# Kernel optimization log

Hardware: AMD Instinct MI355X
Metric: run time of the kernel (lower is better)

## Reference

```python
import jax, jax.numpy as jnp
import numpy as np
import math

C = 768          # in_channels
KC = 768         # key_channels
VC = 768         # value_channels
H = 12           # head_count
B, N = 8, 2048


def setup_inputs() -> dict:
    key = jax.random.key(0)
    ks = jax.random.split(key, 9)
    s = 0.02
    return {
        "x": jax.random.normal(ks[0], (B, N, C), dtype=jnp.float32),
        # Linear weights stored as (in, out); y = x @ W + b
        "Wq": jax.random.normal(ks[1], (C, KC), dtype=jnp.float32) * s,
        "bq": jnp.zeros((KC,), dtype=jnp.float32),
        "Wk": jax.random.normal(ks[2], (C, KC), dtype=jnp.float32) * s,
        "bk": jnp.zeros((KC,), dtype=jnp.float32),
        "Wv": jax.random.normal(ks[3], (C, VC), dtype=jnp.float32) * s,
        "bv": jnp.zeros((VC,), dtype=jnp.float32),
        "Wr": jax.random.normal(ks[4], (VC, C), dtype=jnp.float32) * s,
        "br": jnp.zeros((C,), dtype=jnp.float32),
    }


def reference(x, Wq, bq, Wk, bk, Wv, bv, Wr, br):
    b, n, c = x.shape
    dk = KC // H  # head key channels
    dv = VC // H  # head value channels
    q = (x @ Wq + bq).reshape(b, n, H, dk)
    k = (x @ Wk + bk).reshape(b, n, H, dk)
    v = (x @ Wv + bv).reshape(b, n, H, dv)
    # NOTE: original scales by sqrt(N) (sequence length), not sqrt(d_head)
    scores = jnp.einsum("bqhd,bkhd->bhqk", q, k) / math.sqrt(n)
    attn = jax.nn.softmax(scores, axis=-1)
    out = jnp.einsum("bhqk,bkhd->bqhd", attn, v).reshape(b, n, VC)
    # reprojection + relu; dropout is identity in eval mode
    return jax.nn.relu(out @ Wr + br)
```

## Files before the change

### kernel.cpp

```cpp
#include <hip/hip_runtime.h>
#include <math.h>

typedef unsigned short u16;
typedef short short8 __attribute__((ext_vector_type(8)));
typedef float f32x4 __attribute__((ext_vector_type(4)));

#define BATCH 8
#define SEQ   2048
#define CH    768
#define NH    12
#define DH    64
#define BH    (BATCH*NH)
#define MTOT  (BATCH*SEQ)

#if __has_builtin(__builtin_amdgcn_exp2f)
#define EXP2F(x) __builtin_amdgcn_exp2f(x)
#else
#define EXP2F(x) exp2f(x)
#endif

#define GL2L(g, l) __builtin_amdgcn_global_load_lds( \
    (const __attribute__((address_space(1))) void*)(g), \
    (__attribute__((address_space(3))) void*)(l), 16, 0, 0)

#define BARRIER_FULL() asm volatile("s_waitcnt vmcnt(0) lgkmcnt(0)\n\ts_barrier" ::: "memory")
#define BARRIER_LDS()  asm volatile("s_waitcnt lgkmcnt(0)\n\ts_barrier" ::: "memory")

__device__ __forceinline__ float bf2f(u16 u) {
  union { unsigned int i; float f; } v; v.i = ((unsigned int)u) << 16; return v.f;
}
__device__ __forceinline__ u16 f2bf(float f) {
  union { float f; unsigned int i; } v; v.f = f;
  return (u16)((v.i + 0x7fffu + ((v.i >> 16) & 1u)) >> 16);
}

__global__ void sniff_k(const u16* __restrict__ x, int* __restrict__ flag) {
  __shared__ int cnt;
  if (threadIdx.x == 0) cnt = 0;
  __syncthreads();
  int big = 0;
  for (int i = 0; i < 8; ++i) {
    u16 u = x[threadIdx.x + i * 256];
    int e = (u >> 7) & 0xFF;
    if (e >= 0x89) big++;
  }
  atomicAdd(&cnt, big);
  __syncthreads();
  if (threadIdx.x == 0) *flag = (cnt > 4) ? 1 : 0;
}

__global__ __launch_bounds__(256) void cvt_x_k(const void* __restrict__ xin,
                                               u16* __restrict__ xb,
                                               const int* __restrict__ flag) {
  int i4 = (blockIdx.x * 256 + threadIdx.x) * 4;
  if (*flag) {
    float4 f = *(const float4*)((const float*)xin + i4);
    ushort4 o;
    o.x = f2bf(f.x); o.y = f2bf(f.y); o.z = f2bf(f.z); o.w = f2bf(f.w);
    *(ushort4*)(xb + i4) = o;
  } else {
    *(ushort4*)(xb + i4) = *(const ushort4*)((const u16*)xin + i4);
  }
}

__global__ void cvt_bias_k(const void* b0, const void* b1, const void* b2, const void* b3,
                           u16* __restrict__ biasb, const int* __restrict__ flag) {
  int isf = *flag;
  for (int t = threadIdx.x; t < 4 * CH; t += 256) {
    int wz = t / CH, c = t - wz * CH;
    const void* src = (wz == 0) ? b0 : (wz == 1) ? b1 : (wz == 2) ? b2 : b3;
    biasb[t] = isf ? f2bf(((const float*)src)[c]) : ((const u16*)src)[c];
  }
}

__global__ __launch_bounds__(256) void transpose_w4_k(u16* __restrict__ wt,
    const void* w0, const void* w1, const void* w2, const void* w3,
    const int* __restrict__ flag) {
  __shared__ __align__(16) u16 t[64][65];
  const int z = blockIdx.z;
  const void* in = (z == 0) ? w0 : (z == 1) ? w1 : (z == 2) ? w2 : w3;
  u16* out = wt + (size_t)z * CH * CH;
  const int tid = threadIdx.x;
  const int r0 = blockIdx.y * 64, c0 = blockIdx.x * 64;
  const int isf = *flag;
#pragma unroll
  for (int i = 0; i < 16; ++i) {
    int idx = i * 256 + tid;
    int row = idx >> 6, col = idx & 63;
    size_t g = (size_t)(r0 + row) * CH + c0 + col;
    t[row][col] = isf ? f2bf(((const float*)in)[g]) : ((const u16*)in)[g];
  }
  __syncthreads();
#pragma unroll
  for (int i = 0; i < 16; ++i) {
    int idx = i * 256 + tid;
    int orow = idx >> 6, ocol = idx & 63;
    out[(size_t)(c0 + orow) * CH + r0 + ocol] = t[ocol][orow];
  }
}

template <int EPI>
__global__ __launch_bounds__(256) void gemm_bt_k(
    const u16* __restrict__ A, const u16* __restrict__ BtBase,
    const u16* __restrict__ biasb, u16* __restrict__ outBase,
    u16* __restrict__ voutBase, void* __restrict__ finalOut,
    const int* __restrict__ flag, float qscale) {
  const int K = CH;
  const int tid = threadIdx.x;
  const int wv = tid >> 6, lane = tid & 63, quad = lane >> 4, l16 = lane & 15;
  const int wm = (wv >> 1) * 64, wn = (wv & 1) * 64;

  const int id = blockIdx.x;
  const int xcd = id & 7, u = id >> 3;
  int n0, m0, z;
  if (EPI == 0) {
    int n0z = u % 18, yl = u / 18;
    n0 = (n0z % 6) * 128; z = n0z / 6;
    m0 = (xcd + 8 * yl) * 128;
  } else {
    int n0z = u % 6, yl = u / 6;
    n0 = n0z * 128; z = 3;
    m0 = (xcd + 8 * yl) * 128;
  }
  const u16* Bt = BtBase + (size_t)z * CH * CH;
  const u16* bias = biasb + (size_t)z * CH;

  __shared__ __align__(16) u16 As[128 * 64];
  __shared__ __align__(16) u16 Bs[128 * 64];

#define STAGE_AB(kt_) do { \
    _Pragma("unroll") for (int i_ = 0; i_ < 4; ++i_) { \
      int c_ = tid + i_ * 256; \
      int r_ = c_ >> 3; \
      int pg_ = (c_ & 7) ^ (r_ & 7); \
      GL2L(A + (size_t)(m0 + r_) * K + (kt_) + pg_ * 8, As + c_ * 8); \
    } \
    _Pragma("unroll") for (int i_ = 0; i_ < 4; ++i_) { \
      int c_ = tid + i_ * 256; \
      int r_ = c_ >> 3; \
      int pg_ = (c_ & 7) ^ (r_ & 7); \
      GL2L(Bt + (size_t)(n0 + r_) * K + (kt_) + pg_ * 8, Bs + c_ * 8); \
    } } while (0)

  const f32x4 fz4 = {0.f, 0.f, 0.f, 0.f};
  f32x4 acc[4][4];
#pragma unroll
  for (int mt = 0; mt < 4; ++mt)
#pragma unroll
    for (int nt = 0; nt < 4; ++nt) acc[mt][nt] = fz4;

  STAGE_AB(0);

  for (int kt = 0; kt < K; kt += 64) {
    BARRIER_FULL();

    short8 af[4][2], bf[4][2];
#pragma unroll
    for (int mt = 0; mt < 4; ++mt) {
      int r = wm + mt * 16 + l16;
#pragma unroll
      for (int ks = 0; ks < 2; ++ks) {
        int p = (ks * 4 + quad) ^ (r & 7);
        af[mt][ks] = *(const short8*)(As + r * 64 + p * 8);
      }
    }
#pragma unroll
    for (int nt = 0; nt < 4; ++nt) {
      int r = wn + nt * 16 + l16;
#pragma unroll
      for (int ks = 0; ks < 2; ++ks) {
        int p = (ks * 4 + quad) ^ (r & 7);
        bf[nt][ks] = *(const short8*)(Bs + r * 64 + p * 8);
      }
    }
    BARRIER_LDS();
    if (kt + 64 < K) STAGE_AB(kt + 64);

#pragma unroll
    for (int ks = 0; ks < 2; ++ks)
#pragma unroll
      for (int mt = 0; mt < 4; ++mt)
#pragma unroll
        for (int nt = 0; nt < 4; ++nt)
          acc[mt][nt] = __builtin_amdgcn_mfma_f32_16x16x32_bf16(af[mt][ks], bf[nt][ks],
                                                                acc[mt][nt], 0, 0, 0);
  }
#undef STAGE_AB

  const int of32 = (EPI == 1) ? *flag : 0;
#pragma unroll
  for (int mt = 0; mt < 4; ++mt) {
#pragma unroll
    for (int nt = 0; nt < 4; ++nt) {
      int col = n0 + wn + nt * 16 + l16;
      float bv = bf2f(bias[col]);
      int rowb = m0 + wm + mt * 16 + quad * 4;
      if (EPI == 1) {
#pragma unroll
        for (int r = 0; r < 4; ++r) {
          float vv = fmaxf(acc[mt][nt][r] + bv, 0.0f);
          size_t off = (size_t)(rowb + r) * CH + col;
          if (of32) ((float*)finalOut)[off] = vv;
          else      ((u16*)finalOut)[off] = f2bf(vv);
        }
      } else if (z == 2) {
        int b = rowb >> 11, n = rowb & (SEQ - 1);
        int h = col >> 6, d = col & 63;
        int k5 = n & 31;
        int sig = (((k5 & 15) >> 2) << 3) | ((k5 & 16) >> 2);
        int np = (n & ~31) | sig;
        ushort4 pk;
        pk.x = f2bf(acc[mt][nt][0] + bv);
        pk.y = f2bf(acc[mt][nt][1] + bv);
        pk.z = f2bf(acc[mt][nt][2] + bv);
        pk.w = f2bf(acc[mt][nt][3] + bv);
        *(ushort4*)(voutBase + ((size_t)((b * NH + h) * DH + d)) * SEQ + np) = pk;
      } else {
        float sc = (z == 0) ? qscale : 1.0f;
#pragma unroll
        for (int r = 0; r < 4; ++r) {
          float vv = (acc[mt][nt][r] + bv) * sc;
          int row = rowb + r;
          int b = row >> 11, n = row & (SEQ - 1);
          int h = col >> 6, d = col & 63;
          outBase[(size_t)z * BH * SEQ * DH + ((size_t)(b * NH + h) * SEQ + n) * DH + d] = f2bf(vv);
        }
      }
    }
  }
}

__global__ __launch_bounds__(256, 4) void flash_attn_k(
    const u16* __restrict__ Qg, const u16* __restrict__ Kg,
    const u16* __restrict__ Vtg, u16* __restrict__ Og) {
  const int tid = threadIdx.x;
  const int wv = tid >> 6, lane = tid & 63, quad = lane >> 4, l16 = lane & 15;
  const int id = blockIdx.x;
  const int bh = (id & 7) + 8 * (id >> 7);
  const int q0 = ((id >> 3) & 15) * 128;
  const int b = bh / NH, h = bh - b * NH;

  __shared__ __align__(16) u16 smem[16384];

  const f32x4 fz4 = {0.f, 0.f, 0.f, 0.f};

  const u16* Qp = Qg + (size_t)bh * SEQ * DH + (size_t)q0 * DH;
  const u16* Kp = Kg + (size_t)bh * SEQ * DH;
  const u16* Vp = Vtg + (size_t)bh * DH * SEQ;

#pragma unroll
  for (int i = 0; i < 4; ++i) {
    int c = tid + i * 256; int r = c >> 3; int pg = (c & 7) ^ (r & 7);
    GL2L(Qp + (size_t)r * DH + pg * 8, smem + 8192 + c * 8);
  }
#pragma unroll
  for (int i = 0; i < 2; ++i) {
    int c = tid + i * 256; int r = c >> 3; int pg = (c & 7) ^ (r & 7);
    GL2L(Kp + (size_t)r * DH + pg * 8, smem + c * 8);
    GL2L(Vp + (size_t)r * SEQ + pg * 8, smem + 4096 + c * 8);
  }
  __syncthreads();

  short8 qf[2][2];
#pragma unroll
  for (int mt = 0; mt < 2; ++mt) {
    int r = wv * 32 + mt * 16 + l16;
#pragma unroll
    for (int ks = 0; ks < 2; ++ks) {
      int p = (ks * 4 + quad) ^ (r & 7);
      qf[mt][ks] = *(const short8*)(smem + 8192 + r * 64 + p * 8);
    }
  }

  float lsum[2] = {0.f, 0.f};
  f32x4 oacc[2][4];
#pragma unroll
  for (int mt = 0; mt < 2; ++mt)
#pragma unroll
    for (int dt = 0; dt < 4; ++dt) oacc[mt][dt] = fz4;

  int cur = 0;
  for (int k0 = 0; k0 < SEQ; k0 += 64) {
    BARRIER_FULL();
    u16* Ks = smem + cur * 8192;
    u16* Vs = Ks + 4096;
    if (k0 + 64 < SEQ) {
      int k1 = k0 + 64;
      u16* Kn = smem + (cur ^ 1) * 8192;
#pragma unroll
      for (int i = 0; i < 2; ++i) {
        int c = tid + i * 256; int r = c >> 3; int pg = (c & 7) ^ (r & 7);
        GL2L(Kp + (size_t)(k1 + r) * DH + pg * 8, Kn + c * 8);
        GL2L(Vp + (size_t)r * SEQ + k1 + pg * 8, Kn + 4096 + c * 8);
      }
    }

    f32x4 s[2][4];
#pragma unroll
    for (int mt = 0; mt < 2; ++mt)
#pragma unroll
      for (int nt = 0; nt < 4; ++nt) s[mt][nt] = fz4;
#pragma unroll
    for (int nt = 0; nt < 4; ++nt) {
      int r = nt * 16 + l16;
#pragma unroll
      for (int ks = 0; ks < 2; ++ks) {
        int p = (ks * 4 + quad) ^ (r & 7);
        short8 kf = *(const short8*)(Ks + r * 64 + p * 8);
        s[0][nt] = __builtin_amdgcn_mfma_f32_16x16x32_bf16(kf, qf[0][ks], s[0][nt], 0, 0, 0);
        s[1][nt] = __builtin_amdgcn_mfma_f32_16x16x32_bf16(kf, qf[1][ks], s[1][nt], 0, 0, 0);
      }
    }

    short8 pf[2][2];
#pragma unroll
    for (int mt = 0; mt < 2; ++mt) {
#pragma unroll
      for (int ks = 0; ks < 2; ++ks) {
        float p0 = EXP2F(s[mt][2 * ks][0]);
        float p1 = EXP2F(s[mt][2 * ks][1]);
        float p2 = EXP2F(s[mt][2 * ks][2]);
        float p3 = EXP2F(s[mt][2 * ks][3]);
        float p4 = EXP2F(s[mt][2 * ks + 1][0]);
        float p5 = EXP2F(s[mt][2 * ks + 1][1]);
        float p6 = EXP2F(s[mt][2 * ks + 1][2]);
        float p7 = EXP2F(s[mt][2 * ks + 1][3]);
        lsum[mt] += ((p0 + p1) + (p2 + p3)) + ((p4 + p5) + (p6 + p7));
        union { unsigned int u[4]; short8 s8; } cv;
        cv.u[0] = __builtin_amdgcn_perm(__float_as_uint(p1), __float_as_uint(p0), 0x07060302u);
        cv.u[1] = __builtin_amdgcn_perm(__float_as_uint(p3), __float_as_uint(p2), 0x07060302u);
        cv.u[2] = __builtin_amdgcn_perm(__float_as_uint(p5), __float_as_uint(p4), 0x07060302u);
        cv.u[3] = __builtin_amdgcn_perm(__float_as_uint(p7), __float_as_uint(p6), 0x07060302u);
        pf[mt][ks] = cv.s8;
      }
    }

#pragma unroll
    for (int ks = 0; ks < 2; ++ks) {
#pragma unroll
      for (int dt = 0; dt < 4; ++dt) {
        int rv = dt * 16 + l16;
        int p = (ks * 4 + quad) ^ (rv & 7);
        short8 vf = *(const short8*)(Vs + rv * 64 + p * 8);
        oacc[0][dt] = __builtin_amdgcn_mfma_f32_16x16x32_bf16(pf[0][ks], vf, oacc[0][dt], 0, 0, 0);
        oacc[1][dt] = __builtin_amdgcn_mfma_f32_16x16x32_bf16(pf[1][ks], vf, oacc[1][dt], 0, 0, 0);
      }
    }
    cur ^= 1;
  }

#pragma unroll
  for (int mt = 0; mt < 2; ++mt) {
    float v = lsum[mt];
    v += __shfl_xor(v, 16, 64);
    v += __shfl_xor(v, 32, 64);
    lsum[mt] = 1.0f / v;
  }

#pragma unroll
  for (int mt = 0; mt < 2; ++mt)
#pragma unroll
    for (int r = 0; r < 4; ++r) {
      float inv = __shfl(lsum[mt], quad * 4 + r, 16);
      int qi = q0 + wv * 32 + mt * 16 + quad * 4 + r;
      size_t base = ((size_t)(b * SEQ) + qi) * CH + h * DH;
#pragma unroll
      for (int dt = 0; dt < 4; ++dt) {
        int d = dt * 16 + l16;
        Og[base + d] = f2bf(oacc[mt][dt][r] * inv);
      }
    }
}

extern "C" void kernel_launch(void* const* d_in, const int* in_sizes, int n_in,
                              void* d_out, int out_size, void* d_ws, size_t ws_size,
                              hipStream_t stream) {
  const void* x  = d_in[0];
  const void* Wq = d_in[1];
  const void* bq = d_in[2];
  const void* Wk = d_in[3];
  const void* bk = d_in[4];
  const void* Wv = d_in[5];
  const void* bv = d_in[6];
  const void* Wr = d_in[7];
  const void* br = d_in[8];
  u16* ws = (u16*)d_ws;

  const size_t WSZ = (size_t)CH * CH;
  const size_t XSZ = (size_t)MTOT * CH;
  int* flag  = (int*)ws;
  u16* biasb = ws + 8;
  u16* wt    = ws + 4096;
  u16* xb    = wt + 4 * WSZ;
  u16* q     = xb + XSZ;
  u16* k     = q + XSZ;
  u16* vt    = k + XSZ;

  const float qscale = (float)(1.4426950408889634 / sqrt(2048.0));

  sniff_k<<<1, 256, 0, stream>>>((const u16*)x, flag);
  cvt_x_k<<<XSZ / 1024, 256, 0, stream>>>(x, xb, flag);
  cvt_bias_k<<<1, 256, 0, stream>>>(bq, bk, bv, br, biasb, flag);
  transpose_w4_k<<<dim3(12, 12, 4), 256, 0, stream>>>(wt, Wq, Wk, Wv, Wr, flag);
  gemm_bt_k<0><<<dim3(2304), 256, 0, stream>>>(xb, wt, biasb, q, vt, nullptr,
                                               flag, qscale);
  u16* ao = xb;
  flash_attn_k<<<dim3(1536), 256, 0, stream>>>(q, k, vt, ao);
  gemm_bt_k<1><<<dim3(768), 256, 0, stream>>>(ao, wt, biasb, nullptr, nullptr,
                                              d_out, flag, 1.0f);
}
```

Baseline: 344.3 us.

## Double query tile per attention block and merge setup kernels

The flash attention kernel now gives each block 256 query rows, 64 per wave, instead of 128. Each K/V tile loaded into LDS is therefore reused across twice as many queries, and the grid shrinks to 768 blocks. Q fragments are read straight from global memory into registers instead of being staged through LDS. Each KV step is processed in two halves to limit live score registers. Occupancy is lowered to 3 blocks per SM because of the larger register footprint. Separately, the bias conversion is folded into the format-sniffing kernel to remove one launch.

```diff
diff --git a/kernel.cpp b/kernel.cpp
--- a/kernel.cpp
+++ b/kernel.cpp
@@ -26,6 +26,8 @@
 #define BARRIER_FULL() asm volatile("s_waitcnt vmcnt(0) lgkmcnt(0)\n\ts_barrier" ::: "memory")
 #define BARRIER_LDS()  asm volatile("s_waitcnt lgkmcnt(0)\n\ts_barrier" ::: "memory")
 
+#define MFMA16(a, b, c) __builtin_amdgcn_mfma_f32_16x16x32_bf16((a), (b), (c), 0, 0, 0)
+
 __device__ __forceinline__ float bf2f(u16 u) {
   union { unsigned int i; float f; } v; v.i = ((unsigned int)u) << 16; return v.f;
 }
@@ -34,7 +36,9 @@
   return (u16)((v.i + 0x7fffu + ((v.i >> 16) & 1u)) >> 16);
 }
 
-__global__ void sniff_k(const u16* __restrict__ x, int* __restrict__ flag) {
+__global__ void setup_k(const u16* __restrict__ x, int* __restrict__ flag,
+                        const void* b0, const void* b1, const void* b2, const void* b3,
+                        u16* __restrict__ biasb) {
   __shared__ int cnt;
   if (threadIdx.x == 0) cnt = 0;
   __syncthreads();
@@ -46,7 +50,13 @@
   }
   atomicAdd(&cnt, big);
   __syncthreads();
-  if (threadIdx.x == 0) *flag = (cnt > 4) ? 1 : 0;
+  int isf = (cnt > 4) ? 1 : 0;
+  if (threadIdx.x == 0) *flag = isf;
+  for (int t = threadIdx.x; t < 4 * CH; t += 256) {
+    int wz = t / CH, c = t - wz * CH;
+    const void* src = (wz == 0) ? b0 : (wz == 1) ? b1 : (wz == 2) ? b2 : b3;
+    biasb[t] = isf ? f2bf(((const float*)src)[c]) : ((const u16*)src)[c];
+  }
 }
 
 __global__ __launch_bounds__(256) void cvt_x_k(const void* __restrict__ xin,
@@ -60,16 +70,6 @@
     *(ushort4*)(xb + i4) = o;
   } else {
     *(ushort4*)(xb + i4) = *(const ushort4*)((const u16*)xin + i4);
-  }
-}
-
-__global__ void cvt_bias_k(const void* b0, const void* b1, const void* b2, const void* b3,
-                           u16* __restrict__ biasb, const int* __restrict__ flag) {
-  int isf = *flag;
-  for (int t = threadIdx.x; t < 4 * CH; t += 256) {
-    int wz = t / CH, c = t - wz * CH;
-    const void* src = (wz == 0) ? b0 : (wz == 1) ? b1 : (wz == 2) ? b2 : b3;
-    biasb[t] = isf ? f2bf(((const float*)src)[c]) : ((const u16*)src)[c];
   }
 }
 
@@ -230,60 +230,53 @@
   }
 }
 
-__global__ __launch_bounds__(256, 4) void flash_attn_k(
+__global__ __launch_bounds__(256, 3) void flash_attn_k(
     const u16* __restrict__ Qg, const u16* __restrict__ Kg,
     const u16* __restrict__ Vtg, u16* __restrict__ Og) {
   const int tid = threadIdx.x;
   const int wv = tid >> 6, lane = tid & 63, quad = lane >> 4, l16 = lane & 15;
   const int id = blockIdx.x;
-  const int bh = (id & 7) + 8 * (id >> 7);
-  const int q0 = ((id >> 3) & 15) * 128;
+  const int bh = (id & 7) + 8 * (id >> 6);
+  const int q0 = ((id >> 3) & 7) * 256;
   const int b = bh / NH, h = bh - b * NH;
 
   __shared__ __align__(16) u16 smem[16384];
 
   const f32x4 fz4 = {0.f, 0.f, 0.f, 0.f};
 
-  const u16* Qp = Qg + (size_t)bh * SEQ * DH + (size_t)q0 * DH;
+  const u16* Qp = Qg + (size_t)bh * SEQ * DH + (size_t)(q0 + wv * 64) * DH;
   const u16* Kp = Kg + (size_t)bh * SEQ * DH;
   const u16* Vp = Vtg + (size_t)bh * DH * SEQ;
 
-#pragma unroll
-  for (int i = 0; i < 4; ++i) {
-    int c = tid + i * 256; int r = c >> 3; int pg = (c & 7) ^ (r & 7);
-    GL2L(Qp + (size_t)r * DH + pg * 8, smem + 8192 + c * 8);
-  }
 #pragma unroll
   for (int i = 0; i < 2; ++i) {
     int c = tid + i * 256; int r = c >> 3; int pg = (c & 7) ^ (r & 7);
     GL2L(Kp + (size_t)r * DH + pg * 8, smem + c * 8);
     GL2L(Vp + (size_t)r * SEQ + pg * 8, smem + 4096 + c * 8);
   }
+
+  short8 qf[4][2];
+#pragma unroll
+  for (int mt = 0; mt < 4; ++mt) {
+    int r = mt * 16 + l16;
+#pragma unroll
+    for (int ks = 0; ks < 2; ++ks)
+      qf[mt][ks] = *(const short8*)(Qp + (size_t)r * DH + (ks * 4 + quad) * 8);
+  }
   __syncthreads();
 
-  short8 qf[2][2];
-#pragma unroll
-  for (int mt = 0; mt < 2; ++mt) {
-    int r = wv * 32 + mt * 16 + l16;
-#pragma unroll
-    for (int ks = 0; ks < 2; ++ks) {
-      int p = (ks * 4 + quad) ^ (r & 7);
-      qf[mt][ks] = *(const short8*)(smem + 8192 + r * 64 + p * 8);
-    }
-  }
-
-  float lsum[2] = {0.f, 0.f};
-  f32x4 oacc[2][4];
-#pragma unroll
-  for (int mt = 0; mt < 2; ++mt)
+  float lsum[4] = {0.f, 0.f, 0.f, 0.f};
+  f32x4 oacc[4][4];
+#pragma unroll
+  for (int mt = 0; mt < 4; ++mt)
 #pragma unroll
     for (int dt = 0; dt < 4; ++dt) oacc[mt][dt] = fz4;
 
   int cur = 0;
   for (int k0 = 0; k0 < SEQ; k0 += 64) {
     BARRIER_FULL();
-    u16* Ks = smem + cur * 8192;
-    u16* Vs = Ks + 4096;
+    const u16* Ks = smem + cur * 8192;
+    const u16* Vs = Ks + 4096;
     if (k0 + 64 < SEQ) {
       int k1 = k0 + 64;
       u16* Kn = smem + (cur ^ 1) * 8192;
@@ -295,62 +288,64 @@
       }
     }
 
-    f32x4 s[2][4];
-#pragma unroll
-    for (int mt = 0; mt < 2; ++mt)
-#pragma unroll
-      for (int nt = 0; nt < 4; ++nt) s[mt][nt] = fz4;
-#pragma unroll
-    for (int nt = 0; nt < 4; ++nt) {
-      int r = nt * 16 + l16;
+#pragma unroll
+    for (int half = 0; half < 2; ++half) {
+      const int m0t = 2 * half;
+      f32x4 s0[4], s1[4];
+#pragma unroll
+      for (int nt = 0; nt < 4; ++nt) {
+        int r = nt * 16 + l16;
+        int pa = quad ^ (r & 7);
+        int pb = (4 + quad) ^ (r & 7);
+        short8 kf0 = *(const short8*)(Ks + r * 64 + pa * 8);
+        short8 kf1 = *(const short8*)(Ks + r * 64 + pb * 8);
+        s0[nt] = MFMA16(kf0, qf[m0t][0], fz4);
+        s1[nt] = MFMA16(kf0, qf[m0t + 1][0], fz4);
+        s0[nt] = MFMA16(kf1, qf[m0t][1], s0[nt]);
+        s1[nt] = MFMA16(kf1, qf[m0t + 1][1], s1[nt]);
+      }
+
+      short8 pf[2][2];
+#pragma unroll
+      for (int mi = 0; mi < 2; ++mi) {
+        const f32x4* sv = mi ? s1 : s0;
+#pragma unroll
+        for (int ks = 0; ks < 2; ++ks) {
+          float p0 = EXP2F(sv[2 * ks][0]);
+          float p1 = EXP2F(sv[2 * ks][1]);
+          float p2 = EXP2F(sv[2 * ks][2]);
+          float p3 = EXP2F(sv[2 * ks][3]);
+          float p4 = EXP2F(sv[2 * ks + 1][0]);
+          float p5 = EXP2F(sv[2 * ks + 1][1]);
+          float p6 = EXP2F(sv[2 * ks + 1][2]);
+          float p7 = EXP2F(sv[2 * ks + 1][3]);
+          lsum[m0t + mi] += ((p0 + p1) + (p2 + p3)) + ((p4 + p5) + (p6 + p7));
+          union { unsigned int u[4]; short8 s8; } cv;
+          cv.u[0] = __builtin_amdgcn_perm(__float_as_uint(p1), __float_as_uint(p0), 0x07060302u);
+          cv.u[1] = __builtin_amdgcn_perm(__float_as_uint(p3), __float_as_uint(p2), 0x07060302u);
+          cv.u[2] = __builtin_amdgcn_perm(__float_as_uint(p5), __float_as_uint(p4), 0x07060302u);
+          cv.u[3] = __builtin_amdgcn_perm(__float_as_uint(p7), __float_as_uint(p6), 0x07060302u);
+          pf[mi][ks] = cv.s8;
+        }
+      }
+
 #pragma unroll
       for (int ks = 0; ks < 2; ++ks) {
-        int p = (ks * 4 + quad) ^ (r & 7);
-        short8 kf = *(const short8*)(Ks + r * 64 + p * 8);
-        s[0][nt] = __builtin_amdgcn_mfma_f32_16x16x32_bf16(kf, qf[0][ks], s[0][nt], 0, 0, 0);
-        s[1][nt] = __builtin_amdgcn_mfma_f32_16x16x32_bf16(kf, qf[1][ks], s[1][nt], 0, 0, 0);
-      }
-    }
-
-    short8 pf[2][2];
-#pragma unroll
-    for (int mt = 0; mt < 2; ++mt) {
-#pragma unroll
-      for (int ks = 0; ks < 2; ++ks) {
-        float p0 = EXP2F(s[mt][2 * ks][0]);
-        float p1 = EXP2F(s[mt][2 * ks][1]);
-        float p2 = EXP2F(s[mt][2 * ks][2]);
-        float p3 = EXP2F(s[mt][2 * ks][3]);
-        float p4 = EXP2F(s[mt][2 * ks + 1][0]);
-        float p5 = EXP2F(s[mt][2 * ks + 1][1]);
-        float p6 = EXP2F(s[mt][2 * ks + 1][2]);
-        float p7 = EXP2F(s[mt][2 * ks + 1][3]);
-        lsum[mt] += ((p0 + p1) + (p2 + p3)) + ((p4 + p5) + (p6 + p7));
-        union { unsigned int u[4]; short8 s8; } cv;
-        cv.u[0] = __builtin_amdgcn_perm(__float_as_uint(p1), __float_as_uint(p0), 0x07060302u);
-        cv.u[1] = __builtin_amdgcn_perm(__float_as_uint(p3), __float_as_uint(p2), 0x07060302u);
-        cv.u[2] = __builtin_amdgcn_perm(__float_as_uint(p5), __float_as_uint(p4), 0x07060302u);
-        cv.u[3] = __builtin_amdgcn_perm(__float_as_uint(p7), __float_as_uint(p6), 0x07060302u);
-        pf[mt][ks] = cv.s8;
-      }
-    }
-
-#pragma unroll
-    for (int ks = 0; ks < 2; ++ks) {
-#pragma unroll
-      for (int dt = 0; dt < 4; ++dt) {
-        int rv = dt * 16 + l16;
-        int p = (ks * 4 + quad) ^ (rv & 7);
-        short8 vf = *(const short8*)(Vs + rv * 64 + p * 8);
-        oacc[0][dt] = __builtin_amdgcn_mfma_f32_16x16x32_bf16(pf[0][ks], vf, oacc[0][dt], 0, 0, 0);
-        oacc[1][dt] = __builtin_amdgcn_mfma_f32_16x16x32_bf16(pf[1][ks], vf, oacc[1][dt], 0, 0, 0);
+#pragma unroll
+        for (int dt = 0; dt < 4; ++dt) {
+          int rv = dt * 16 + l16;
+          int p = (ks * 4 + quad) ^ (rv & 7);
+          short8 vf = *(const short8*)(Vs + rv * 64 + p * 8);
+          oacc[m0t][dt] = MFMA16(pf[0][ks], vf, oacc[m0t][dt]);
+          oacc[m0t + 1][dt] = MFMA16(pf[1][ks], vf, oacc[m0t + 1][dt]);
+        }
       }
     }
     cur ^= 1;
   }
 
 #pragma unroll
-  for (int mt = 0; mt < 2; ++mt) {
+  for (int mt = 0; mt < 4; ++mt) {
     float v = lsum[mt];
     v += __shfl_xor(v, 16, 64);
     v += __shfl_xor(v, 32, 64);
@@ -358,11 +353,11 @@
   }
 
 #pragma unroll
-  for (int mt = 0; mt < 2; ++mt)
+  for (int mt = 0; mt < 4; ++mt)
 #pragma unroll
     for (int r = 0; r < 4; ++r) {
       float inv = __shfl(lsum[mt], quad * 4 + r, 16);
-      int qi = q0 + wv * 32 + mt * 16 + quad * 4 + r;
+      int qi = q0 + wv * 64 + mt * 16 + quad * 4 + r;
       size_t base = ((size_t)(b * SEQ) + qi) * CH + h * DH;
 #pragma unroll
       for (int dt = 0; dt < 4; ++dt) {
@@ -398,14 +393,13 @@
 
   const float qscale = (float)(1.4426950408889634 / sqrt(2048.0));
 
-  sniff_k<<<1, 256, 0, stream>>>((const u16*)x, flag);
+  setup_k<<<1, 256, 0, stream>>>((const u16*)x, flag, bq, bk, bv, br, biasb);
   cvt_x_k<<<XSZ / 1024, 256, 0, stream>>>(x, xb, flag);
-  cvt_bias_k<<<1, 256, 0, stream>>>(bq, bk, bv, br, biasb, flag);
   transpose_w4_k<<<dim3(12, 12, 4), 256, 0, stream>>>(wt, Wq, Wk, Wv, Wr, flag);
   gemm_bt_k<0><<<dim3(2304), 256, 0, stream>>>(xb, wt, biasb, q, vt, nullptr,
                                                flag, qscale);
   u16* ao = xb;
-  flash_attn_k<<<dim3(1536), 256, 0, stream>>>(q, k, vt, ao);
+  flash_attn_k<<<dim3(768), 256, 0, stream>>>(q, k, vt, ao);
   gemm_bt_k<1><<<dim3(768), 256, 0, stream>>>(ao, wt, biasb, nullptr, nullptr,
                                               d_out, flag, 1.0f);
 }
```

Result: slower. 422.6 us (+22.7%).

## Compute softmax row sums via MFMA with ones, add setprio, merge setup kernels

Applied to the files above, without the earlier changes.

In the flash attention loop, the per-lane float row-sum accumulation is replaced by MFMA products of the bf16 probability fragments with a ones vector. This moves the reduction onto the matrix units and drops the end-of-kernel shuffle reduction. MFMA sections are wrapped in s_setprio to favour wave issue, and the bias conversion kernel is folded into the sniff kernel to save a launch. The sums now use bf16-rounded probabilities, which matches the numerator but adds four extra MFMAs per tile.

```diff
diff --git a/kernel.cpp b/kernel.cpp
--- a/kernel.cpp
+++ b/kernel.cpp
@@ -26,6 +26,8 @@
 #define BARRIER_FULL() asm volatile("s_waitcnt vmcnt(0) lgkmcnt(0)\n\ts_barrier" ::: "memory")
 #define BARRIER_LDS()  asm volatile("s_waitcnt lgkmcnt(0)\n\ts_barrier" ::: "memory")
 
+#define MFMA16(a, b, c) __builtin_amdgcn_mfma_f32_16x16x32_bf16((a), (b), (c), 0, 0, 0)
+
 __device__ __forceinline__ float bf2f(u16 u) {
   union { unsigned int i; float f; } v; v.i = ((unsigned int)u) << 16; return v.f;
 }
@@ -34,7 +36,9 @@
   return (u16)((v.i + 0x7fffu + ((v.i >> 16) & 1u)) >> 16);
 }
 
-__global__ void sniff_k(const u16* __restrict__ x, int* __restrict__ flag) {
+__global__ void setup_k(const u16* __restrict__ x, int* __restrict__ flag,
+                        const void* b0, const void* b1, const void* b2, const void* b3,
+                        u16* __restrict__ biasb) {
   __shared__ int cnt;
   if (threadIdx.x == 0) cnt = 0;
   __syncthreads();
@@ -46,7 +50,13 @@
   }
   atomicAdd(&cnt, big);
   __syncthreads();
-  if (threadIdx.x == 0) *flag = (cnt > 4) ? 1 : 0;
+  int isf = (cnt > 4) ? 1 : 0;
+  if (threadIdx.x == 0) *flag = isf;
+  for (int t = threadIdx.x; t < 4 * CH; t += 256) {
+    int wz = t / CH, c = t - wz * CH;
+    const void* src = (wz == 0) ? b0 : (wz == 1) ? b1 : (wz == 2) ? b2 : b3;
+    biasb[t] = isf ? f2bf(((const float*)src)[c]) : ((const u16*)src)[c];
+  }
 }
 
 __global__ __launch_bounds__(256) void cvt_x_k(const void* __restrict__ xin,
@@ -60,16 +70,6 @@
     *(ushort4*)(xb + i4) = o;
   } else {
     *(ushort4*)(xb + i4) = *(const ushort4*)((const u16*)xin + i4);
-  }
-}
-
-__global__ void cvt_bias_k(const void* b0, const void* b1, const void* b2, const void* b3,
-                           u16* __restrict__ biasb, const int* __restrict__ flag) {
-  int isf = *flag;
-  for (int t = threadIdx.x; t < 4 * CH; t += 256) {
-    int wz = t / CH, c = t - wz * CH;
-    const void* src = (wz == 0) ? b0 : (wz == 1) ? b1 : (wz == 2) ? b2 : b3;
-    biasb[t] = isf ? f2bf(((const float*)src)[c]) : ((const u16*)src)[c];
   }
 }
 
@@ -243,6 +243,8 @@
   __shared__ __align__(16) u16 smem[16384];
 
   const f32x4 fz4 = {0.f, 0.f, 0.f, 0.f};
+  const short8 ones = {(short)0x3F80, (short)0x3F80, (short)0x3F80, (short)0x3F80,
+                       (short)0x3F80, (short)0x3F80, (short)0x3F80, (short)0x3F80};
 
   const u16* Qp = Qg + (size_t)bh * SEQ * DH + (size_t)q0 * DH;
   const u16* Kp = Kg + (size_t)bh * SEQ * DH;
@@ -272,8 +274,9 @@
     }
   }
 
-  float lsum[2] = {0.f, 0.f};
+  f32x4 sumacc[2];
   f32x4 oacc[2][4];
+  sumacc[0] = fz4; sumacc[1] = fz4;
 #pragma unroll
   for (int mt = 0; mt < 2; ++mt)
 #pragma unroll
@@ -282,8 +285,8 @@
   int cur = 0;
   for (int k0 = 0; k0 < SEQ; k0 += 64) {
     BARRIER_FULL();
-    u16* Ks = smem + cur * 8192;
-    u16* Vs = Ks + 4096;
+    const u16* Ks = smem + cur * 8192;
+    const u16* Vs = Ks + 4096;
     if (k0 + 64 < SEQ) {
       int k1 = k0 + 64;
       u16* Kn = smem + (cur ^ 1) * 8192;
@@ -300,6 +303,7 @@
     for (int mt = 0; mt < 2; ++mt)
 #pragma unroll
       for (int nt = 0; nt < 4; ++nt) s[mt][nt] = fz4;
+    __builtin_amdgcn_s_setprio(1);
 #pragma unroll
     for (int nt = 0; nt < 4; ++nt) {
       int r = nt * 16 + l16;
@@ -311,6 +315,7 @@
         s[1][nt] = __builtin_amdgcn_mfma_f32_16x16x32_bf16(kf, qf[1][ks], s[1][nt], 0, 0, 0);
       }
     }
+    __builtin_amdgcn_s_setprio(0);
 
     short8 pf[2][2];
 #pragma unroll
@@ -325,7 +330,6 @@
         float p5 = EXP2F(s[mt][2 * ks + 1][1]);
         float p6 = EXP2F(s[mt][2 * ks + 1][2]);
         float p7 = EXP2F(s[mt][2 * ks + 1][3]);
-        lsum[mt] += ((p0 + p1) + (p2 + p3)) + ((p4 + p5) + (p6 + p7));
         union { unsigned int u[4]; short8 s8; } cv;
         cv.u[0] = __builtin_amdgcn_perm(__float_as_uint(p1), __float_as_uint(p0), 0x07060302u);
         cv.u[1] = __builtin_amdgcn_perm(__float_as_uint(p3), __float_as_uint(p2), 0x07060302u);
@@ -335,6 +339,11 @@
       }
     }
 
+    __builtin_amdgcn_s_setprio(1);
+    sumacc[0] = MFMA16(pf[0][0], ones, sumacc[0]);
+    sumacc[1] = MFMA16(pf[1][0], ones, sumacc[1]);
+    sumacc[0] = MFMA16(pf[0][1], ones, sumacc[0]);
+    sumacc[1] = MFMA16(pf[1][1], ones, sumacc[1]);
 #pragma unroll
     for (int ks = 0; ks < 2; ++ks) {
 #pragma unroll
@@ -346,22 +355,15 @@
         oacc[1][dt] = __builtin_amdgcn_mfma_f32_16x16x32_bf16(pf[1][ks], vf, oacc[1][dt], 0, 0, 0);
       }
     }
+    __builtin_amdgcn_s_setprio(0);
     cur ^= 1;
   }
 
 #pragma unroll
-  for (int mt = 0; mt < 2; ++mt) {
-    float v = lsum[mt];
-    v += __shfl_xor(v, 16, 64);
-    v += __shfl_xor(v, 32, 64);
-    lsum[mt] = 1.0f / v;
-  }
-
-#pragma unroll
   for (int mt = 0; mt < 2; ++mt)
 #pragma unroll
     for (int r = 0; r < 4; ++r) {
-      float inv = __shfl(lsum[mt], quad * 4 + r, 16);
+      float inv = 1.0f / sumacc[mt][r];
       int qi = q0 + wv * 32 + mt * 16 + quad * 4 + r;
       size_t base = ((size_t)(b * SEQ) + qi) * CH + h * DH;
 #pragma unroll
@@ -398,9 +400,8 @@
 
   const float qscale = (float)(1.4426950408889634 / sqrt(2048.0));
 
-  sniff_k<<<1, 256, 0, stream>>>((const u16*)x, flag);
+  setup_k<<<1, 256, 0, stream>>>((const u16*)x, flag, bq, bk, bv, br, biasb);
   cvt_x_k<<<XSZ / 1024, 256, 0, stream>>>(x, xb, flag);
-  cvt_bias_k<<<1, 256, 0, stream>>>(bq, bk, bv, br, biasb, flag);
   transpose_w4_k<<<dim3(12, 12, 4), 256, 0, stream>>>(wt, Wq, Wk, Wv, Wr, flag);
   gemm_bt_k<0><<<dim3(2304), 256, 0, stream>>>(xb, wt, biasb, q, vt, nullptr,
                                                flag, qscale);
```

Measured after the change: 322.2 us. -6.4%, faster.
